# Optimization experiments

Measured on AMD Instinct MI355X. Metric: run time of the kernel, lower is better.

## Reference

```python
import jax, jax.numpy as jnp
import numpy as np

EPS = 1e-12  # matches torch F.normalize default eps


def _l2_normalize(x, axis=-1):
    norm = jnp.sqrt(jnp.sum(x * x, axis=axis, keepdims=True))
    return x / jnp.maximum(norm, EPS)


def setup_inputs() -> dict:
    key = jax.random.key(0)
    k1, k2 = jax.random.split(key)
    B, D, P = 8192, 512, 32768
    z_context = jax.random.normal(k1, (B, D), dtype=jnp.float32)
    prototypes = jax.random.normal(k2, (P, D), dtype=jnp.float32) * 0.02
    return {"z_context": z_context, "prototypes": prototypes, "topk": 3}


def reference(z_context, prototypes, topk):
    # Cosine similarity: normalize queries and prototype bank, then GEMM.
    z_norm = _l2_normalize(z_context, axis=-1)          # [B, D]
    p_norm = _l2_normalize(prototypes, axis=-1)         # [P, D]
    sim = jnp.einsum('bd,pd->bp', z_norm, p_norm)       # [B, P]
    k = min(topk, prototypes.shape[0])
    topk_val, topk_idx = jax.lax.top_k(sim, k)          # [B, k] each
    return sim, topk_idx, topk_val
```

## Files before the change

### kernel.cpp

```cpp
#include <hip/hip_runtime.h>
#include <float.h>
#include <stdint.h>

#define D_DIM 512

typedef __attribute__((ext_vector_type(8))) short bf16x8;
typedef __attribute__((ext_vector_type(4))) float f32x4;

#define GLD_LDS16(g, l)                                              \
    __builtin_amdgcn_global_load_lds(                                \
        (const __attribute__((address_space(1))) void*)(g),          \
        (__attribute__((address_space(3))) void*)(l), 16, 0, 0)

__device__ __forceinline__ uint32_t pk_bf16(float a, float b) {
    uint32_t ua = __builtin_bit_cast(uint32_t, a) + 0x8000u;
    uint32_t ub = __builtin_bit_cast(uint32_t, b) + 0x8000u;
    return (ua >> 16) | (ub & 0xFFFF0000u);
}

__global__ __launch_bounds__(256) void convert_norm_kernel(
        const float* __restrict__ X, unsigned short* __restrict__ Xb,
        float* __restrict__ r, int R) {
    int row = blockIdx.x * 4 + (threadIdx.x >> 6);
    if (row >= R) return;
    int lane = threadIdx.x & 63;
    const float* x = X + (size_t)row * D_DIM + lane * 8;
    float4 f0 = *(const float4*)(x);
    float4 f1 = *(const float4*)(x + 4);
    float s = f0.x*f0.x + f0.y*f0.y + f0.z*f0.z + f0.w*f0.w
            + f1.x*f1.x + f1.y*f1.y + f1.z*f1.z + f1.w*f1.w;
#pragma unroll
    for (int off = 32; off; off >>= 1) s += __shfl_xor(s, off);
    float rv = 1.0f / fmaxf(sqrtf(s), 1e-12f);
    if (lane == 0) r[row] = rv;
    uint4 w;
    w.x = pk_bf16(f0.x * rv, f0.y * rv);
    w.y = pk_bf16(f0.z * rv, f0.w * rv);
    w.z = pk_bf16(f1.x * rv, f1.y * rv);
    w.w = pk_bf16(f1.z * rv, f1.w * rv);
    *(uint4*)(Xb + (size_t)row * D_DIM + lane * 8) = w;
}

template <bool FUSE>
__global__ __launch_bounds__(256) void gemm_lds_bf16(
        const unsigned short* __restrict__ Zb,
        const unsigned short* __restrict__ Pb,
        float* __restrict__ sim, uint2* __restrict__ part, int Pn) {
    constexpr int SH_BYTES = FUSE ? 43008 : 32768;
    __shared__ __align__(16) unsigned char SH[SH_BYTES];
    uint4* S = (uint4*)SH;

    int bi = blockIdx.x;
    int mb, nb;
    if (gridDim.x == 16384) {
        int xcd = bi & 7;
        int r = bi >> 3;
        mb = xcd * 8 + (r & 7);
        nb = r >> 3;
    } else {
        nb = bi % (Pn / 128);
        mb = bi / (Pn / 128);
    }
    const int bm = mb * 128, bn = nb * 128;

    const int tid = threadIdx.x;
    const int lane = tid & 63;
    const int wid = tid >> 6;
    const int wr = wid >> 1, wc = wid & 1;
    const int ln15 = lane & 15, hi = lane >> 4;

    const unsigned short* gA[4];
    const unsigned short* gB[4];
    int ldsIdx[4];
#pragma unroll
    for (int q = 0; q < 4; ++q) {
        int flat = q * 256 + tid;
        int row = flat >> 3;
        int c = flat & 7;
        int cg = c ^ (row & 7);
        gA[q] = Zb + (size_t)(bm + row) * D_DIM + cg * 8;
        gB[q] = Pb + (size_t)(bn + row) * D_DIM + cg * 8;
        ldsIdx[q] = flat;
    }

    f32x4 acc[4][4] = {};

#pragma unroll 1
    for (int s8 = 0; s8 < 8; ++s8) {
#pragma unroll
        for (int q = 0; q < 4; ++q) {
            GLD_LDS16(gA[q], &S[ldsIdx[q]]);
            GLD_LDS16(gB[q], &S[1024 + ldsIdx[q]]);
            gA[q] += 64;
            gB[q] += 64;
        }
        asm volatile("s_waitcnt vmcnt(0)" ::: "memory");
        __syncthreads();

#pragma unroll
        for (int kk = 0; kk < 2; ++kk) {
            bf16x8 av[4], bv[4];
            const int kch = kk * 4 + hi;
#pragma unroll
            for (int t = 0; t < 4; ++t) {
                int arow = wr * 64 + t * 16 + ln15;
                av[t] = __builtin_bit_cast(bf16x8,
                        S[arow * 8 + (kch ^ (arow & 7))]);
                int brow = wc * 64 + t * 16 + ln15;
                bv[t] = __builtin_bit_cast(bf16x8,
                        S[1024 + brow * 8 + (kch ^ (brow & 7))]);
            }
#pragma unroll
            for (int i = 0; i < 4; ++i)
#pragma unroll
                for (int j = 0; j < 4; ++j)
                    acc[i][j] = __builtin_amdgcn_mfma_f32_16x16x32_bf16(
                        av[i], bv[j], acc[i][j], 0, 0, 0);
        }
        __syncthreads();
    }

#pragma unroll
    for (int i = 0; i < 4; ++i) {
#pragma unroll
        for (int rr = 0; rr < 4; ++rr) {
            int row = bm + wr * 64 + i * 16 + hi * 4 + rr;
#pragma unroll
            for (int j = 0; j < 4; ++j) {
                int col = bn + wc * 64 + j * 16 + ln15;
                sim[(size_t)row * Pn + col] = acc[i][j][rr];
            }
        }
    }

    if constexpr (FUSE) {
        float* T = (float*)SH;
        uint2* M = (uint2*)(SH + 34816);
        const int NB = Pn >> 7;
        const int r = tid & 63;
        const int q = wid;
#pragma unroll 1
        for (int hf = 0; hf < 2; ++hf) {
            __syncthreads();
            if (wr == hf) {
#pragma unroll
                for (int i = 0; i < 4; ++i)
#pragma unroll
                    for (int j = 0; j < 4; ++j)
                        *(f32x4*)&T[(wc * 64 + j * 16 + ln15) * 68 + i * 16 + hi * 4]
                            = acc[i][j];
            }
            __syncthreads();
            float tv[4]; int ti[4];
#pragma unroll
            for (int k = 0; k < 4; ++k) { tv[k] = -FLT_MAX; ti[k] = 0x7FFFFFFF; }
#pragma unroll
            for (int c = 0; c < 32; ++c) {
                float val = T[(q * 32 + c) * 68 + r];
                if (val > tv[3]) {
                    int p = 3;
#pragma unroll
                    for (int j2 = 2; j2 >= 0; --j2)
                        if (val > tv[j2]) { tv[j2+1] = tv[j2]; ti[j2+1] = ti[j2]; p = j2; }
                    tv[p] = val; ti[p] = bn + q * 32 + c;
                }
            }
#pragma unroll
            for (int k = 0; k < 4; ++k)
                M[q * 256 + k * 64 + r] =
                    make_uint2(__builtin_bit_cast(uint32_t, tv[k]), (uint32_t)ti[k]);
            __syncthreads();
            if (tid < 64) {
                float fv[4]; int fi[4];
#pragma unroll
                for (int k = 0; k < 4; ++k) { fv[k] = -FLT_MAX; fi[k] = 0x7FFFFFFF; }
#pragma unroll
                for (int qq = 0; qq < 4; ++qq)
#pragma unroll
                    for (int k = 0; k < 4; ++k) {
                        uint2 u = M[qq * 256 + k * 64 + tid];
                        float val = __builtin_bit_cast(float, u.x);
                        if (val > fv[3]) {
                            int p = 3;
#pragma unroll
                            for (int j2 = 2; j2 >= 0; --j2)
                                if (val > fv[j2]) { fv[j2+1] = fv[j2]; fi[j2+1] = fi[j2]; p = j2; }
                            fv[p] = val; fi[p] = (int)u.y;
                        }
                    }
                size_t o = ((size_t)(bm + hf * 64 + tid) * NB + nb) * 4;
#pragma unroll
                for (int k = 0; k < 4; ++k)
                    part[o + k] =
                        make_uint2(__builtin_bit_cast(uint32_t, fv[k]), (uint32_t)fi[k]);
            }
        }
    }
}

__global__ __launch_bounds__(256) void topk_reduce(const uint2* __restrict__ part,
        const float* __restrict__ Z, const float* __restrict__ Pm,
        const float* __restrict__ rz, const float* __restrict__ rp,
        float* __restrict__ oidx, float* __restrict__ oval, int Pn) {
    int row = blockIdx.x * 4 + (threadIdx.x >> 6);
    int lane = threadIdx.x & 63;
    const int NB = Pn >> 7;
    const uint2* pr = part + (size_t)row * NB * 4;

    float v[8]; int ix[8];
#pragma unroll
    for (int j = 0; j < 8; ++j) { v[j] = -FLT_MAX; ix[j] = -1; }

    const int total = NB * 4;
    for (int c = lane; c < total; c += 64) {
        uint2 u = pr[c];
        float val = __builtin_bit_cast(float, u.x);
        if (val > v[7]) {
            int idx = (int)u.y;
            int pos = 7;
#pragma unroll
            for (int j = 6; j >= 0; --j) {
                if (val > v[j]) { v[j+1] = v[j]; ix[j+1] = ix[j]; pos = j; }
            }
            v[pos] = val; ix[pos] = idx;
        }
    }

    int cand[8];
#pragma unroll
    for (int k = 0; k < 8; ++k) {
        float bv = v[0]; int bi2 = ix[0];
#pragma unroll
        for (int off = 32; off; off >>= 1) {
            float ov = __shfl_xor(bv, off);
            int oi = __shfl_xor(bi2, off);
            if (ov > bv || (ov == bv && oi >= 0 && (unsigned)oi < (unsigned)bi2)) {
                bv = ov; bi2 = oi;
            }
        }
        cand[k] = bi2;
        if (bi2 == ix[0]) {
#pragma unroll
            for (int j = 0; j < 7; ++j) { v[j] = v[j+1]; ix[j] = ix[j+1]; }
            v[7] = -FLT_MAX; ix[7] = -1;
        }
    }

    float zv[8];
    const float* zrow = Z + (size_t)row * D_DIM + lane * 8;
#pragma unroll
    for (int j = 0; j < 8; ++j) zv[j] = zrow[j];
    float rzv = rz[row];

    float ex[8];
#pragma unroll
    for (int c = 0; c < 8; ++c) {
        int idx = cand[c];
        const float* prow = Pm + (size_t)idx * D_DIM + lane * 8;
        float s = 0.f;
#pragma unroll
        for (int j = 0; j < 8; ++j) s += zv[j] * prow[j];
#pragma unroll
        for (int off = 32; off; off >>= 1) s += __shfl_xor(s, off);
        ex[c] = s * rzv * rp[idx];
    }

    bool used[8] = {};
#pragma unroll
    for (int k = 0; k < 3; ++k) {
        float bv = -FLT_MAX; int bi2 = Pn; int bc = 0;
#pragma unroll
        for (int c = 0; c < 8; ++c) {
            if (!used[c] && (ex[c] > bv || (ex[c] == bv && cand[c] < bi2))) {
                bv = ex[c]; bi2 = cand[c]; bc = c;
            }
        }
        used[bc] = true;
        if (lane == 0) {
            oidx[(size_t)row * 3 + k] = (float)bi2;
            oval[(size_t)row * 3 + k] = bv;
        }
    }
}

__global__ __launch_bounds__(256) void rnorm_kernel(const float* __restrict__ X,
                                                    float* __restrict__ r, int R) {
    int row = blockIdx.x * 4 + (threadIdx.x >> 6);
    if (row >= R) return;
    int lane = threadIdx.x & 63;
    const float* x = X + (size_t)row * D_DIM;
    float s = 0.f;
#pragma unroll
    for (int t = 0; t < 2; ++t) {
        float4 v = *(const float4*)(x + (t * 64 + lane) * 4);
        s += v.x * v.x + v.y * v.y + v.z * v.z + v.w * v.w;
    }
#pragma unroll
    for (int off = 32; off; off >>= 1) s += __shfl_xor(s, off);
    if (lane == 0) r[row] = 1.0f / fmaxf(sqrtf(s), 1e-12f);
}

__global__ __launch_bounds__(256, 2) void gemm_bf16_sim(const float* __restrict__ Z,
        const float* __restrict__ Pm, const float* __restrict__ rz,
        const float* __restrict__ rp, float* __restrict__ sim, int Pn) {
    __shared__ uint4 As16[1024];
    __shared__ uint4 Bs16[1024];
    int bi = blockIdx.x;
    int mb, nb;
    if (gridDim.x == 16384) {
        int xcd = bi & 7;
        int r = bi >> 3;
        mb = xcd * 8 + (r & 7);
        nb = r >> 3;
    } else {
        nb = bi % (Pn / 128);
        mb = bi / (Pn / 128);
    }
    const int bm = mb * 128, bn = nb * 128;
    const int tid = threadIdx.x;
    const int srow = tid >> 1;
    const int half = tid & 1;
    const float* aP = Z  + (size_t)(bm + srow) * D_DIM + half * 32;
    const float* bP = Pm + (size_t)(bn + srow) * D_DIM + half * 32;
    const int lane = tid & 63;
    const int wid = tid >> 6;
    const int wr = wid >> 1, wc = wid & 1;
    const int ln15 = lane & 15, hi = lane >> 4;
    f32x4 acc[4][4] = {};
    float4 f[8], g[8];
#pragma unroll
    for (int q = 0; q < 8; ++q) {
        f[q] = *(const float4*)(aP + q * 4);
        g[q] = *(const float4*)(bP + q * 4);
    }
#pragma unroll 1
    for (int s = 0; s < 8; ++s) {
#pragma unroll
        for (int q8 = 0; q8 < 4; ++q8) {
            uint4 wa, wb;
            wa.x = pk_bf16(f[2*q8].x,   f[2*q8].y);
            wa.y = pk_bf16(f[2*q8].z,   f[2*q8].w);
            wa.z = pk_bf16(f[2*q8+1].x, f[2*q8+1].y);
            wa.w = pk_bf16(f[2*q8+1].z, f[2*q8+1].w);
            wb.x = pk_bf16(g[2*q8].x,   g[2*q8].y);
            wb.y = pk_bf16(g[2*q8].z,   g[2*q8].w);
            wb.z = pk_bf16(g[2*q8+1].x, g[2*q8+1].y);
            wb.w = pk_bf16(g[2*q8+1].z, g[2*q8+1].w);
            int colByte = half * 64 + q8 * 16;
            int idx = srow * 8 + ((colByte ^ ((srow & 7) << 4)) >> 4);
            As16[idx] = wa;
            Bs16[idx] = wb;
        }
        __syncthreads();
        if (s < 7) {
            int k0 = (s + 1) * 64;
#pragma unroll
            for (int q = 0; q < 8; ++q) {
                f[q] = *(const float4*)(aP + k0 + q * 4);
                g[q] = *(const float4*)(bP + k0 + q * 4);
            }
        }
#pragma unroll
        for (int kk = 0; kk < 2; ++kk) {
            bf16x8 av[4], bv[4];
            const int cb = kk * 64 + hi * 16;
#pragma unroll
            for (int t = 0; t < 4; ++t) {
                int arow = wr * 64 + t * 16 + ln15;
                av[t] = __builtin_bit_cast(bf16x8,
                        As16[arow * 8 + ((cb ^ ((arow & 7) << 4)) >> 4)]);
                int brow = wc * 64 + t * 16 + ln15;
                bv[t] = __builtin_bit_cast(bf16x8,
                        Bs16[brow * 8 + ((cb ^ ((brow & 7) << 4)) >> 4)]);
            }
#pragma unroll
            for (int i = 0; i < 4; ++i)
#pragma unroll
                for (int j = 0; j < 4; ++j)
                    acc[i][j] = __builtin_amdgcn_mfma_f32_16x16x32_bf16(
                        av[i], bv[j], acc[i][j], 0, 0, 0);
        }
        __syncthreads();
    }
    float rpv[4];
#pragma unroll
    for (int j = 0; j < 4; ++j) rpv[j] = rp[bn + wc * 64 + j * 16 + ln15];
#pragma unroll
    for (int i = 0; i < 4; ++i) {
#pragma unroll
        for (int rr = 0; rr < 4; ++rr) {
            int row = bm + wr * 64 + i * 16 + hi * 4 + rr;
            float rzv = rz[row];
#pragma unroll
            for (int j = 0; j < 4; ++j) {
                int col = bn + wc * 64 + j * 16 + ln15;
                sim[(size_t)row * Pn + col] = acc[i][j][rr] * rzv * rpv[j];
            }
        }
    }
}

__global__ __launch_bounds__(256) void topk_refine(const float* __restrict__ sim,
        const float* __restrict__ Z, const float* __restrict__ Pm,
        const float* __restrict__ rz, const float* __restrict__ rp,
        float* __restrict__ oidx, float* __restrict__ oval, int Pn) {
    int row = blockIdx.x * 4 + (threadIdx.x >> 6);
    int lane = threadIdx.x & 63;
    const float* rptr = sim + (size_t)row * Pn;

    float v[8]; int ix[8];
#pragma unroll
    for (int j = 0; j < 8; ++j) { v[j] = -FLT_MAX; ix[j] = -1; }

    const int iters = Pn >> 8;
    for (int t = 0; t < iters; ++t) {
        int base = t * 256 + lane * 4;
        float4 q = *(const float4*)(rptr + base);
        float vals[4] = {q.x, q.y, q.z, q.w};
#pragma unroll
        for (int e = 0; e < 4; ++e) {
            float val = vals[e];
            if (val > v[7]) {
                int idx = base + e;
                int pos = 7;
#pragma unroll
                for (int j = 6; j >= 0; --j) {
                    if (val > v[j]) { v[j+1] = v[j]; ix[j+1] = ix[j]; pos = j; }
                }
                v[pos] = val; ix[pos] = idx;
            }
        }
    }

    int cand[8];
#pragma unroll
    for (int k = 0; k < 8; ++k) {
        float bv = v[0]; int bi2 = ix[0];
#pragma unroll
        for (int off = 32; off; off >>= 1) {
            float ov = __shfl_xor(bv, off);
            int oi = __shfl_xor(bi2, off);
            if (ov > bv || (ov == bv && oi >= 0 && (unsigned)oi < (unsigned)bi2)) {
                bv = ov; bi2 = oi;
            }
        }
        cand[k] = bi2;
        if (bi2 == ix[0]) {
#pragma unroll
            for (int j = 0; j < 7; ++j) { v[j] = v[j+1]; ix[j] = ix[j+1]; }
            v[7] = -FLT_MAX; ix[7] = -1;
        }
    }

    float zv[8];
    const float* zrow = Z + (size_t)row * D_DIM + lane * 8;
#pragma unroll
    for (int j = 0; j < 8; ++j) zv[j] = zrow[j];
    float rzv = rz[row];

    float ex[8];
#pragma unroll
    for (int c = 0; c < 8; ++c) {
        int idx = cand[c];
        const float* prow = Pm + (size_t)idx * D_DIM + lane * 8;
        float s = 0.f;
#pragma unroll
        for (int j = 0; j < 8; ++j) s += zv[j] * prow[j];
#pragma unroll
        for (int off = 32; off; off >>= 1) s += __shfl_xor(s, off);
        ex[c] = s * rzv * rp[idx];
    }

    bool used[8] = {};
#pragma unroll
    for (int k = 0; k < 3; ++k) {
        float bv = -FLT_MAX; int bi2 = Pn; int bc = 0;
#pragma unroll
        for (int c = 0; c < 8; ++c) {
            if (!used[c] && (ex[c] > bv || (ex[c] == bv && cand[c] < bi2))) {
                bv = ex[c]; bi2 = cand[c]; bc = c;
            }
        }
        used[bc] = true;
        if (lane == 0) {
            oidx[(size_t)row * 3 + k] = (float)bi2;
            oval[(size_t)row * 3 + k] = bv;
        }
    }
}

extern "C" void kernel_launch(void* const* d_in, const int* in_sizes, int n_in,
                              void* d_out, int out_size, void* d_ws, size_t ws_size,
                              hipStream_t stream) {
    const float* Z  = (const float*)d_in[0];
    const float* Pm = (const float*)d_in[1];
    const int B  = in_sizes[0] / D_DIM;
    const int Pn = in_sizes[1] / D_DIM;

    float* sim  = (float*)d_out;
    float* oidx = sim + (size_t)B * Pn;
    float* oval = oidx + (size_t)B * 3;

    float* rz = (float*)d_ws;
    float* rp = rz + B;
    unsigned short* Zb = (unsigned short*)(rp + Pn);
    unsigned short* Pb = Zb + (size_t)B * D_DIM;
    uint2* part = (uint2*)(Pb + (size_t)Pn * D_DIM);

    const size_t NB = (size_t)Pn / 128;
    const size_t need_bf16  = (size_t)(B + Pn) * 4 + (size_t)(B + Pn) * D_DIM * 2;
    const size_t need_fused = need_bf16 + (size_t)B * NB * 4 * sizeof(uint2);

    dim3 grid((B / 128) * (Pn / 128));

    if (ws_size >= need_fused) {
        convert_norm_kernel<<<B / 4, 256, 0, stream>>>(Z, Zb, rz, B);
        convert_norm_kernel<<<Pn / 4, 256, 0, stream>>>(Pm, Pb, rp, Pn);
        gemm_lds_bf16<true><<<grid, 256, 0, stream>>>(Zb, Pb, sim, part, Pn);
        topk_reduce<<<B / 4, 256, 0, stream>>>(part, Z, Pm, rz, rp, oidx, oval, Pn);
    } else if (ws_size >= need_bf16) {
        convert_norm_kernel<<<B / 4, 256, 0, stream>>>(Z, Zb, rz, B);
        convert_norm_kernel<<<Pn / 4, 256, 0, stream>>>(Pm, Pb, rp, Pn);
        gemm_lds_bf16<false><<<grid, 256, 0, stream>>>(Zb, Pb, sim, nullptr, Pn);
        topk_refine<<<B / 4, 256, 0, stream>>>(sim, Z, Pm, rz, rp, oidx, oval, Pn);
    } else {
        rnorm_kernel<<<B / 4, 256, 0, stream>>>(Z, rz, B);
        rnorm_kernel<<<Pn / 4, 256, 0, stream>>>(Pm, rp, Pn);
        gemm_bf16_sim<<<grid, 256, 0, stream>>>(Z, Pm, rz, rp, sim, Pn);
        topk_refine<<<B / 4, 256, 0, stream>>>(sim, Z, Pm, rz, rp, oidx, oval, Pn);
    }
}
```

Baseline: 745.9 us.

## Double-buffer LDS tiles in GEMM mainloop and batch top-k candidate checks

Shared memory is doubled to two buffers so each K-step's global-to-LDS loads are issued before computing on the previous buffer. The loop now waits on a partial vmcnt and uses raw s_barrier with wave priority hints, which lets memory latency overlap with MFMA work. The fused top-k scan now loads four candidates at once and skips the insertion path when their max cannot enter the list. The 64KB static LDS allocation may reduce occupancy.

```diff
diff --git a/kernel.cpp b/kernel.cpp
--- a/kernel.cpp
+++ b/kernel.cpp
@@ -46,8 +46,7 @@
         const unsigned short* __restrict__ Zb,
         const unsigned short* __restrict__ Pb,
         float* __restrict__ sim, uint2* __restrict__ part, int Pn) {
-    constexpr int SH_BYTES = FUSE ? 43008 : 32768;
-    __shared__ __align__(16) unsigned char SH[SH_BYTES];
+    __shared__ __align__(16) unsigned char SH[65536];
     uint4* S = (uint4*)SH;
 
     int bi = blockIdx.x;
@@ -85,18 +84,35 @@
 
     f32x4 acc[4][4] = {};
 
+#pragma unroll
+    for (int q = 0; q < 4; ++q) {
+        GLD_LDS16(gA[q], &S[ldsIdx[q]]);
+        GLD_LDS16(gB[q], &S[1024 + ldsIdx[q]]);
+        gA[q] += 64;
+        gB[q] += 64;
+    }
+
+    int cur = 0;
 #pragma unroll 1
     for (int s8 = 0; s8 < 8; ++s8) {
-#pragma unroll
-        for (int q = 0; q < 4; ++q) {
-            GLD_LDS16(gA[q], &S[ldsIdx[q]]);
-            GLD_LDS16(gB[q], &S[1024 + ldsIdx[q]]);
-            gA[q] += 64;
-            gB[q] += 64;
-        }
-        asm volatile("s_waitcnt vmcnt(0)" ::: "memory");
-        __syncthreads();
-
+        const int nxt = cur ^ 1;
+        if (s8 < 7) {
+#pragma unroll
+            for (int q = 0; q < 4; ++q) {
+                GLD_LDS16(gA[q], &S[nxt * 2048 + ldsIdx[q]]);
+                GLD_LDS16(gB[q], &S[nxt * 2048 + 1024 + ldsIdx[q]]);
+                gA[q] += 64;
+                gB[q] += 64;
+            }
+            asm volatile("s_waitcnt vmcnt(8)" ::: "memory");
+        } else {
+            asm volatile("s_waitcnt vmcnt(0)" ::: "memory");
+        }
+        __builtin_amdgcn_s_barrier();
+        __builtin_amdgcn_sched_barrier(0);
+
+        const int sb = cur * 2048;
+        __builtin_amdgcn_s_setprio(1);
 #pragma unroll
         for (int kk = 0; kk < 2; ++kk) {
             bf16x8 av[4], bv[4];
@@ -105,10 +121,10 @@
             for (int t = 0; t < 4; ++t) {
                 int arow = wr * 64 + t * 16 + ln15;
                 av[t] = __builtin_bit_cast(bf16x8,
-                        S[arow * 8 + (kch ^ (arow & 7))]);
+                        S[sb + arow * 8 + (kch ^ (arow & 7))]);
                 int brow = wc * 64 + t * 16 + ln15;
                 bv[t] = __builtin_bit_cast(bf16x8,
-                        S[1024 + brow * 8 + (kch ^ (brow & 7))]);
+                        S[sb + 1024 + brow * 8 + (kch ^ (brow & 7))]);
             }
 #pragma unroll
             for (int i = 0; i < 4; ++i)
@@ -117,7 +133,10 @@
                     acc[i][j] = __builtin_amdgcn_mfma_f32_16x16x32_bf16(
                         av[i], bv[j], acc[i][j], 0, 0, 0);
         }
-        __syncthreads();
+        __builtin_amdgcn_s_setprio(0);
+        __builtin_amdgcn_sched_barrier(0);
+        __builtin_amdgcn_s_barrier();
+        cur = nxt;
     }
 
 #pragma unroll
@@ -155,14 +174,25 @@
 #pragma unroll
             for (int k = 0; k < 4; ++k) { tv[k] = -FLT_MAX; ti[k] = 0x7FFFFFFF; }
 #pragma unroll
-            for (int c = 0; c < 32; ++c) {
-                float val = T[(q * 32 + c) * 68 + r];
-                if (val > tv[3]) {
-                    int p = 3;
-#pragma unroll
-                    for (int j2 = 2; j2 >= 0; --j2)
-                        if (val > tv[j2]) { tv[j2+1] = tv[j2]; ti[j2+1] = ti[j2]; p = j2; }
-                    tv[p] = val; ti[p] = bn + q * 32 + c;
+            for (int c4 = 0; c4 < 32; c4 += 4) {
+                float e0 = T[(q * 32 + c4 + 0) * 68 + r];
+                float e1 = T[(q * 32 + c4 + 1) * 68 + r];
+                float e2 = T[(q * 32 + c4 + 2) * 68 + r];
+                float e3 = T[(q * 32 + c4 + 3) * 68 + r];
+                float mg = fmaxf(fmaxf(e0, e1), fmaxf(e2, e3));
+                if (mg > tv[3]) {
+                    float ee[4] = {e0, e1, e2, e3};
+#pragma unroll
+                    for (int e = 0; e < 4; ++e) {
+                        float val = ee[e];
+                        if (val > tv[3]) {
+                            int p = 3;
+#pragma unroll
+                            for (int j2 = 2; j2 >= 0; --j2)
+                                if (val > tv[j2]) { tv[j2+1] = tv[j2]; ti[j2+1] = ti[j2]; p = j2; }
+                            tv[p] = val; ti[p] = bn + q * 32 + c4 + e;
+                        }
+                    }
                 }
             }
 #pragma unroll
```

Measured after the change: 765.7 us. +2.7%, slower.
